# Kernel tuning notes

Hardware: AMD Instinct MI355X
Metric: run time of the kernel (lower is better)

The kernel has to match this reference:

```python
import jax, jax.numpy as jnp
import numpy as np

ALPHA = 0.5
EPS = 1e-12

def _l2norm(v):
    return v / (jnp.linalg.norm(v) + EPS)

def _spectral_norm_weight(W, u):
    # torch spectral_norm forward (training, n_power_iterations=1):
    # one power iteration with detached u, v; sigma = u' @ W @ v; W_sn = W / sigma
    v = jax.lax.stop_gradient(_l2norm(W.T @ u))          # [in]
    u2 = jax.lax.stop_gradient(_l2norm(W @ v))           # [out]
    sigma = u2 @ (W @ v)
    return W / sigma


def setup_inputs() -> dict:
    key = jax.random.key(0)
    ks = jax.random.split(key, 12)
    B, D_IN, D_H, D_OUT = 256, 1024, 2048, 1000

    def xavier(k, shape, gain):
        fan_out, fan_in = shape
        a = gain * np.sqrt(6.0 / (fan_in + fan_out))
        return jax.random.uniform(k, shape, jnp.float32, -a, a)

    x = jax.random.normal(ks[0], (B, D_IN), jnp.float32)
    # W_in: nn.Linear default init (kaiming-uniform-ish); plain uniform is fine for a reference
    lim_in = 1.0 / np.sqrt(D_IN)
    W_in_w = jax.random.uniform(ks[1], (D_H, D_IN), jnp.float32, -lim_in, lim_in)
    W_in_b = jax.random.uniform(ks[2], (D_H,), jnp.float32, -lim_in, lim_in)
    u = jax.random.normal(ks[3], (D_H,), jnp.float32)  # spectral-norm power-iteration vector

    W0 = xavier(ks[4], (D_H, D_H), 0.8)
    W1 = xavier(ks[5], (D_H, D_H), 0.8)
    W2 = xavier(ks[6], (D_H, D_H), 0.8)
    b0 = jnp.zeros((D_H,), jnp.float32)
    b1 = jnp.zeros((D_H,), jnp.float32)
    b2 = jnp.zeros((D_H,), jnp.float32)

    lim_h = 1.0 / np.sqrt(D_H)
    head_w = jax.random.uniform(ks[7], (D_OUT, D_H), jnp.float32, -lim_h, lim_h)
    head_b = jax.random.uniform(ks[8], (D_OUT,), jnp.float32, -lim_h, lim_h)

    return {"x": x, "W_in_w": W_in_w, "W_in_b": W_in_b, "u": u,
            "W0": W0, "b0": b0, "W1": W1, "b1": b1, "W2": W2, "b2": b2,
            "head_w": head_w, "head_b": head_b, "steps": 30}


def reference(x, W_in_w, W_in_b, u, W0, b0, W1, b1, W2, b2, head_w, head_b, steps):
    W_in_sn = _spectral_norm_weight(W_in_w, u)
    x_proj = x @ W_in_sn.T + W_in_b                      # [B, D_H], constant across steps
    layers = ((W0, b0), (W1, b1), (W2, b2))

    def step(h, _):
        for W, b in layers:
            h = (1.0 - ALPHA) * h + ALPHA * jnp.tanh(x_proj + h @ W.T + b)
        return h, None

    h0 = jnp.zeros((x.shape[0], W0.shape[0]), x.dtype)
    h, _ = jax.lax.scan(step, h0, None, length=steps)
    return h @ head_w.T + head_b
```

## Files before the change

### kernel.cpp

```cpp
#include <hip/hip_runtime.h>
#include <hip/hip_fp16.h>
#include <math.h>

typedef _Float16 h16;
typedef __attribute__((ext_vector_type(8))) _Float16 half8;
typedef __attribute__((ext_vector_type(4))) float f32x4;

#define GLOAD_LDS16(gp, lp) __builtin_amdgcn_global_load_lds( \
    (const __attribute__((address_space(1))) void*)(gp),      \
    (__attribute__((address_space(3))) void*)(lp), 16, 0, 0)

union SmemGemm3 {
  h16   buf[3][96 * 128];
  float red[4][2048];
};

__device__ __forceinline__ void stage3(SmemGemm3& sm, int bi,
                                       const h16* __restrict__ Ag,
                                       const h16* __restrict__ Bg,
                                       int kk, int kdim, int wave, int lane) {
  h16* As = sm.buf[bi];
  h16* Bs = As + 32 * 128;
  const int kb = kk * 128;
#pragma unroll
  for (int i = 0; i < 2; ++i) {
    const int id = wave * 2 + i;
    const int chunk = id * 64 + lane;
    const int r = chunk >> 4, cg = chunk & 15;
    GLOAD_LDS16(Ag + (long)r * kdim + kb + ((cg ^ (r & 7)) << 3),
                As + id * 512);
  }
#pragma unroll
  for (int i = 0; i < 4; ++i) {
    const int id = wave * 4 + i;
    const int chunk = id * 64 + lane;
    const int r = chunk >> 4, cg = chunk & 15;
    GLOAD_LDS16(Bg + (long)r * kdim + kb + ((cg ^ (r & 7)) << 3),
                Bs + id * 512);
  }
}

template <int KDIM>
__device__ __forceinline__ void gemm_core3(SmemGemm3& sm,
                                           const h16* __restrict__ Ag,
                                           const h16* __restrict__ Bg,
                                           int wave, int lane) {
  f32x4 acc[2][4];
#pragma unroll
  for (int a = 0; a < 2; ++a)
#pragma unroll
    for (int c = 0; c < 4; ++c) acc[a][c] = (f32x4){0.f, 0.f, 0.f, 0.f};

  const int mr = lane & 15, q = lane >> 4;
  const int kg = wave * 4 + q;
  const int ro = ((kg ^ (mr & 7)) << 3);
  constexpr int NIT = KDIM / 128;
  stage3(sm, 0, Ag, Bg, 0, KDIM, wave, lane);
  stage3(sm, 1, Ag, Bg, 1, KDIM, wave, lane);
#pragma unroll
  for (int kk = 0; kk < NIT; ++kk) {
    if (kk + 2 < NIT) {
      stage3(sm, (kk + 2) % 3, Ag, Bg, kk + 2, KDIM, wave, lane);
      asm volatile("s_waitcnt vmcnt(12)" ::: "memory");
    } else if (kk + 2 == NIT) {
      asm volatile("s_waitcnt vmcnt(6)" ::: "memory");
    } else {
      asm volatile("s_waitcnt vmcnt(0)" ::: "memory");
    }
    __builtin_amdgcn_s_barrier();
    const h16* As = sm.buf[kk % 3];
    const h16* Bs = As + 32 * 128;
    half8 a0 = *(const half8*)(As + mr * 128 + ro);
    half8 a1 = *(const half8*)(As + (mr + 16) * 128 + ro);
#pragma unroll
    for (int fc = 0; fc < 4; ++fc) {
      half8 bv = *(const half8*)(Bs + (fc * 16 + mr) * 128 + ro);
      acc[0][fc] = __builtin_amdgcn_mfma_f32_16x16x32_f16(a0, bv, acc[0][fc], 0, 0, 0);
      acc[1][fc] = __builtin_amdgcn_mfma_f32_16x16x32_f16(a1, bv, acc[1][fc], 0, 0, 0);
    }
    asm volatile("s_waitcnt lgkmcnt(0)" ::: "memory");
    __builtin_amdgcn_s_barrier();
  }
  __syncthreads();
#pragma unroll
  for (int fr = 0; fr < 2; ++fr)
#pragma unroll
    for (int fc = 0; fc < 4; ++fc)
#pragma unroll
      for (int r = 0; r < 4; ++r)
        sm.red[wave][(fr * 16 + q * 4 + r) * 64 + fc * 16 + mr] = acc[fr][fc][r];
  __syncthreads();
}

__device__ __forceinline__ float fast_tanh(float x) {
  float e = __expf(2.0f * fabsf(x));
  float t = 1.0f - 2.0f / (e + 1.0f);
  return copysignf(t, x);
}

__global__ void k_zero(float* tbuf, float* sbuf) {
  const int t = threadIdx.x;
  tbuf[t] = 0.f;
  if (t < 2) sbuf[t] = 0.f;
}

__global__ void __launch_bounds__(256)
k_prep1(const float* __restrict__ Win, const float* __restrict__ u,
        float* __restrict__ t) {
  const int kc = blockIdx.x & 3, jc = blockIdx.x >> 2;
  const int k = kc * 256 + threadIdx.x;
  const int j0 = jc * 64;
  float acc = 0.f;
#pragma unroll 4
  for (int j = 0; j < 64; ++j)
    acc = fmaf(Win[(long)(j0 + j) * 1024 + k], u[j0 + j], acc);
  atomicAdd(&t[k], acc);
}

__global__ void __launch_bounds__(256)
k_prep1b(const float* __restrict__ t, float* __restrict__ sbuf) {
  const int k = blockIdx.x * 256 + threadIdx.x;
  float v = t[k];
  float p = v * v;
#pragma unroll
  for (int off = 32; off > 0; off >>= 1) p += __shfl_down(p, off);
  if ((threadIdx.x & 63) == 0) atomicAdd(&sbuf[0], p);
}

__global__ void __launch_bounds__(256)
k_prep2(const float* __restrict__ Win, const float* __restrict__ t,
        float* __restrict__ sbuf) {
  const int row = blockIdx.x * 4 + (threadIdx.x >> 6);
  const int lane = threadIdx.x & 63;
  float acc = 0.f;
  for (int kk = lane; kk < 1024; kk += 64)
    acc = fmaf(Win[row * 1024 + kk], t[kk], acc);
#pragma unroll
  for (int off = 32; off > 0; off >>= 1) acc += __shfl_down(acc, off);
  if (lane == 0) atomicAdd(&sbuf[1], acc * acc);
}

__global__ void __launch_bounds__(256)
k_cvt(const float* __restrict__ W0, const float* __restrict__ W1,
      const float* __restrict__ W2, const float* __restrict__ Win,
      const float* __restrict__ Hw, const float* __restrict__ X,
      h16* __restrict__ w16, h16* __restrict__ wi16,
      h16* __restrict__ hw16, h16* __restrict__ x16) {
  const long e = (long)(blockIdx.x * 256 + threadIdx.x) * 8;
  const float* src; h16* dst;
  if (e < 4194304)       { src = W0 + e;              dst = w16 + e; }
  else if (e < 8388608)  { src = W1 + (e - 4194304);  dst = w16 + e; }
  else if (e < 12582912) { src = W2 + (e - 8388608);  dst = w16 + e; }
  else if (e < 14680064) { src = Win + (e - 12582912); dst = wi16 + (e - 12582912); }
  else if (e < 16728064) { src = Hw + (e - 14680064);  dst = hw16 + (e - 14680064); }
  else if (e < 16777216) {
    half8 z = (half8){};
    *(half8*)(hw16 + 2048000 + (e - 16728064)) = z;
    return;
  }
  else                   { src = X + (e - 16777216);   dst = x16 + (e - 16777216); }
  f32x4 f0 = *(const f32x4*)src, f1 = *(const f32x4*)(src + 4);
  half8 h;
#pragma unroll
  for (int i = 0; i < 4; ++i) { h[i] = (h16)f0[i]; h[i + 4] = (h16)f1[i]; }
  *(half8*)dst = h;
}

__global__ void __launch_bounds__(256)
k_xproj(const h16* __restrict__ x16, const h16* __restrict__ wi16,
        const float* __restrict__ Winb, const float* __restrict__ sbuf,
        float* __restrict__ xp, float* __restrict__ h32, h16* __restrict__ h16a) {
  __shared__ SmemGemm3 sm;
  const int rb = blockIdx.x >> 5, cb = blockIdx.x & 31;
  const int wave = threadIdx.x >> 6, lane = threadIdx.x & 63;
  gemm_core3<1024>(sm, x16 + rb * 32 * 1024, wi16 + (long)cb * 64 * 1024, wave, lane);
  const float inv_sigma = sqrtf(sbuf[0] / sbuf[1]);
  const int e = threadIdx.x * 8;
  const int gi = rb * 32 + (e >> 6), gj = cb * 64 + (e & 63);
  const long base = (long)gi * 2048 + gj;
  f32x4 s0 = *(const f32x4*)&sm.red[0][e], s1 = *(const f32x4*)&sm.red[0][e + 4];
#pragma unroll
  for (int w = 1; w < 4; ++w) {
    s0 += *(const f32x4*)&sm.red[w][e];
    s1 += *(const f32x4*)&sm.red[w][e + 4];
  }
  f32x4 b0v = *(const f32x4*)&Winb[gj], b1v = *(const f32x4*)&Winb[gj + 4];
  f32x4 v0 = s0 * inv_sigma + b0v, v1 = s1 * inv_sigma + b1v;
  *(f32x4*)&xp[base] = v0; *(f32x4*)&xp[base + 4] = v1;
  f32x4 zz = (f32x4){0.f, 0.f, 0.f, 0.f};
  *(f32x4*)&h32[base] = zz; *(f32x4*)&h32[base + 4] = zz;
  half8 hz = (half8){};
  *(half8*)&h16a[base] = hz;
}

__global__ void __launch_bounds__(256)
k_layer(const h16* __restrict__ hin, const h16* __restrict__ W,
        const float* __restrict__ bl, const float* __restrict__ xp,
        float* __restrict__ h32, h16* __restrict__ hout) {
  __shared__ SmemGemm3 sm;
  const int rb = blockIdx.x >> 5, cb = blockIdx.x & 31;
  const int wave = threadIdx.x >> 6, lane = threadIdx.x & 63;
  gemm_core3<2048>(sm, hin + rb * 32 * 2048, W + (long)cb * 64 * 2048, wave, lane);
  const int e = threadIdx.x * 8;
  const int gi = rb * 32 + (e >> 6), gj = cb * 64 + (e & 63);
  const long base = (long)gi * 2048 + gj;
  f32x4 s0 = *(const f32x4*)&sm.red[0][e], s1 = *(const f32x4*)&sm.red[0][e + 4];
#pragma unroll
  for (int w = 1; w < 4; ++w) {
    s0 += *(const f32x4*)&sm.red[w][e];
    s1 += *(const f32x4*)&sm.red[w][e + 4];
  }
  f32x4 xp0 = *(const f32x4*)&xp[base], xp1 = *(const f32x4*)&xp[base + 4];
  f32x4 b0v = *(const f32x4*)&bl[gj],   b1v = *(const f32x4*)&bl[gj + 4];
  f32x4 ho0 = *(const f32x4*)&h32[base], ho1 = *(const f32x4*)&h32[base + 4];
  f32x4 z0 = xp0 + s0 + b0v, z1 = xp1 + s1 + b1v;
  f32x4 hn0, hn1; half8 hh;
#pragma unroll
  for (int i = 0; i < 4; ++i) {
    hn0[i] = 0.5f * ho0[i] + 0.5f * fast_tanh(z0[i]);
    hn1[i] = 0.5f * ho1[i] + 0.5f * fast_tanh(z1[i]);
    hh[i] = (h16)hn0[i]; hh[i + 4] = (h16)hn1[i];
  }
  *(f32x4*)&h32[base] = hn0; *(f32x4*)&h32[base + 4] = hn1;
  *(half8*)&hout[base] = hh;
}

__global__ void __launch_bounds__(256)
k_head(const h16* __restrict__ hf, const h16* __restrict__ hw16,
       const float* __restrict__ hb, float* __restrict__ out) {
  __shared__ SmemGemm3 sm;
  const int rb = blockIdx.x >> 4, cb = blockIdx.x & 15;
  const int wave = threadIdx.x >> 6, lane = threadIdx.x & 63;
  gemm_core3<2048>(sm, hf + rb * 32 * 2048, hw16 + (long)cb * 64 * 2048, wave, lane);
  const int e = threadIdx.x * 8;
  const int gi = rb * 32 + (e >> 6), gj = cb * 64 + (e & 63);
  f32x4 s0 = *(const f32x4*)&sm.red[0][e], s1 = *(const f32x4*)&sm.red[0][e + 4];
#pragma unroll
  for (int w = 1; w < 4; ++w) {
    s0 += *(const f32x4*)&sm.red[w][e];
    s1 += *(const f32x4*)&sm.red[w][e + 4];
  }
#pragma unroll
  for (int i = 0; i < 4; ++i) {
    int j0 = gj + i;
    if (j0 < 1000) out[(long)gi * 1000 + j0] = s0[i] + hb[j0];
    int j1 = gj + 4 + i;
    if (j1 < 1000) out[(long)gi * 1000 + j1] = s1[i] + hb[j1];
  }
}

#define OFF_W16   0L
#define OFF_WI16  25165824L
#define OFF_X16   29360128L
#define OFF_HW16  29884416L
#define OFF_XP    34078720L
#define OFF_H32   36175872L
#define OFF_H16A  38273024L
#define OFF_H16B  39321600L
#define OFF_T     40370176L
#define OFF_S     40374272L

extern "C" void kernel_launch(void* const* d_in, const int* in_sizes, int n_in,
                              void* d_out, int out_size, void* d_ws, size_t ws_size,
                              hipStream_t stream) {
  const float* x     = (const float*)d_in[0];
  const float* Win_w = (const float*)d_in[1];
  const float* Win_b = (const float*)d_in[2];
  const float* u     = (const float*)d_in[3];
  const float* W0    = (const float*)d_in[4];
  const float* b0    = (const float*)d_in[5];
  const float* W1    = (const float*)d_in[6];
  const float* b1    = (const float*)d_in[7];
  const float* W2    = (const float*)d_in[8];
  const float* b2    = (const float*)d_in[9];
  const float* headw = (const float*)d_in[10];
  const float* headb = (const float*)d_in[11];

  char* ws = (char*)d_ws;
  h16*   w16  = (h16*)(ws + OFF_W16);
  h16*   wi16 = (h16*)(ws + OFF_WI16);
  h16*   x16  = (h16*)(ws + OFF_X16);
  h16*   hw16 = (h16*)(ws + OFF_HW16);
  float* xp   = (float*)(ws + OFF_XP);
  float* h32  = (float*)(ws + OFF_H32);
  h16*   h16a = (h16*)(ws + OFF_H16A);
  h16*   h16b = (h16*)(ws + OFF_H16B);
  float* tbuf = (float*)(ws + OFF_T);
  float* sbuf = (float*)(ws + OFF_S);

  k_zero<<<1, 1024, 0, stream>>>(tbuf, sbuf);
  k_prep1<<<128, 256, 0, stream>>>(Win_w, u, tbuf);
  k_prep1b<<<4, 256, 0, stream>>>(tbuf, sbuf);
  k_prep2<<<512, 256, 0, stream>>>(Win_w, tbuf, sbuf);
  k_cvt<<<8320, 256, 0, stream>>>(W0, W1, W2, Win_w, headw, x, w16, wi16, hw16, x16);
  k_xproj<<<256, 256, 0, stream>>>(x16, wi16, Win_b, sbuf, xp, h32, h16a);

  const h16*   wptr[3] = {w16, w16 + 4194304, w16 + 8388608};
  const float* bptr[3] = {b0, b1, b2};
  h16* hbuf[2] = {h16a, h16b};
  for (int s = 0; s < 30; ++s) {
    for (int l = 0; l < 3; ++l) {
      const int d = s * 3 + l;
      k_layer<<<256, 256, 0, stream>>>(hbuf[d & 1], wptr[l], bptr[l], xp, h32,
                                       hbuf[(d + 1) & 1]);
    }
  }
  k_head<<<128, 256, 0, stream>>>(hbuf[0], hw16, headb, (float*)d_out);
}
```

Measured before the change: 997.0 us.

## Fuse 90 layer launches into one persistent kernel with row-block barriers

Replaces 90 separate layer kernel launches with a single persistent kernel. Blocks sharing a 32-row batch slice synchronize through atomic counters in global memory, one counter per row block. The fp32 hidden state now stays in registers across steps instead of making a round trip through global memory, and the first layer skips its GEMM because h0 is zero. This removes launch overhead and the h32 traffic, but it relies on all 256 blocks being co-resident and adds spin-wait barrier costs.

```diff
diff --git a/kernel.cpp b/kernel.cpp
--- a/kernel.cpp
+++ b/kernel.cpp
@@ -98,10 +98,78 @@
   return copysignf(t, x);
 }
 
-__global__ void k_zero(float* tbuf, float* sbuf) {
+__global__ void __launch_bounds__(256)
+k_layers90(const h16* __restrict__ w16, const float* __restrict__ xp,
+           const float* __restrict__ b0v, const float* __restrict__ b1v,
+           const float* __restrict__ b2v, h16* __restrict__ ha,
+           h16* __restrict__ hb, unsigned* __restrict__ csync) {
+  __shared__ SmemGemm3 sm;
+  const int rb = blockIdx.x >> 5, cb = blockIdx.x & 31;
+  const int wave = threadIdx.x >> 6, lane = threadIdx.x & 63;
+  const int e = threadIdx.x * 8;
+  const int gi = rb * 32 + (e >> 6), gj = cb * 64 + (e & 63);
+  const long obase = (long)gi * 2048 + gj;
+  const f32x4 xpA = *(const f32x4*)&xp[obase];
+  const f32x4 xpB = *(const f32x4*)&xp[obase + 4];
+  f32x4 hA, hB;
+  half8 hh;
+
+  {
+    f32x4 z0 = xpA + *(const f32x4*)&b0v[gj];
+    f32x4 z1 = xpB + *(const f32x4*)&b0v[gj + 4];
+#pragma unroll
+    for (int i = 0; i < 4; ++i) {
+      hA[i] = 0.5f * fast_tanh(z0[i]);
+      hB[i] = 0.5f * fast_tanh(z1[i]);
+      hh[i] = (h16)hA[i]; hh[i + 4] = (h16)hB[i];
+    }
+    *(half8*)&hb[obase] = hh;
+  }
+
+#pragma unroll 1
+  for (int d = 1; d < 90; ++d) {
+    asm volatile("s_waitcnt vmcnt(0)" ::: "memory");
+    __syncthreads();
+    if (threadIdx.x == 0) {
+      __builtin_amdgcn_fence(__ATOMIC_RELEASE, "agent");
+      atomicAdd(&csync[rb], 1u);
+      while (__hip_atomic_load(&csync[rb], __ATOMIC_RELAXED,
+                               __HIP_MEMORY_SCOPE_AGENT) < (unsigned)(d * 32))
+        __builtin_amdgcn_s_sleep(2);
+      __builtin_amdgcn_fence(__ATOMIC_ACQUIRE, "agent");
+    }
+    __syncthreads();
+
+    const int L = d % 3;
+    const h16* W = w16 + (long)L * 4194304;
+    const float* bl = (L == 0) ? b0v : (L == 1) ? b1v : b2v;
+    const h16* hin = (d & 1) ? hb : ha;
+    h16* hout = (d & 1) ? ha : hb;
+    gemm_core3<2048>(sm, hin + rb * 32 * 2048, W + (long)cb * 64 * 2048,
+                     wave, lane);
+    f32x4 s0 = *(const f32x4*)&sm.red[0][e], s1 = *(const f32x4*)&sm.red[0][e + 4];
+#pragma unroll
+    for (int w = 1; w < 4; ++w) {
+      s0 += *(const f32x4*)&sm.red[w][e];
+      s1 += *(const f32x4*)&sm.red[w][e + 4];
+    }
+    f32x4 z0 = s0 + xpA + *(const f32x4*)&bl[gj];
+    f32x4 z1 = s1 + xpB + *(const f32x4*)&bl[gj + 4];
+#pragma unroll
+    for (int i = 0; i < 4; ++i) {
+      hA[i] = 0.5f * hA[i] + 0.5f * fast_tanh(z0[i]);
+      hB[i] = 0.5f * hB[i] + 0.5f * fast_tanh(z1[i]);
+      hh[i] = (h16)hA[i]; hh[i + 4] = (h16)hB[i];
+    }
+    *(half8*)&hout[obase] = hh;
+  }
+}
+
+__global__ void k_zero(float* tbuf, float* sbuf, unsigned* csync) {
   const int t = threadIdx.x;
   tbuf[t] = 0.f;
   if (t < 2) sbuf[t] = 0.f;
+  if (t < 8) csync[t] = 0u;
 }
 
 __global__ void __launch_bounds__(256)
@@ -169,7 +237,7 @@
 __global__ void __launch_bounds__(256)
 k_xproj(const h16* __restrict__ x16, const h16* __restrict__ wi16,
         const float* __restrict__ Winb, const float* __restrict__ sbuf,
-        float* __restrict__ xp, float* __restrict__ h32, h16* __restrict__ h16a) {
+        float* __restrict__ xp) {
   __shared__ SmemGemm3 sm;
   const int rb = blockIdx.x >> 5, cb = blockIdx.x & 31;
   const int wave = threadIdx.x >> 6, lane = threadIdx.x & 63;
@@ -187,42 +255,6 @@
   f32x4 b0v = *(const f32x4*)&Winb[gj], b1v = *(const f32x4*)&Winb[gj + 4];
   f32x4 v0 = s0 * inv_sigma + b0v, v1 = s1 * inv_sigma + b1v;
   *(f32x4*)&xp[base] = v0; *(f32x4*)&xp[base + 4] = v1;
-  f32x4 zz = (f32x4){0.f, 0.f, 0.f, 0.f};
-  *(f32x4*)&h32[base] = zz; *(f32x4*)&h32[base + 4] = zz;
-  half8 hz = (half8){};
-  *(half8*)&h16a[base] = hz;
-}
-
-__global__ void __launch_bounds__(256)
-k_layer(const h16* __restrict__ hin, const h16* __restrict__ W,
-        const float* __restrict__ bl, const float* __restrict__ xp,
-        float* __restrict__ h32, h16* __restrict__ hout) {
-  __shared__ SmemGemm3 sm;
-  const int rb = blockIdx.x >> 5, cb = blockIdx.x & 31;
-  const int wave = threadIdx.x >> 6, lane = threadIdx.x & 63;
-  gemm_core3<2048>(sm, hin + rb * 32 * 2048, W + (long)cb * 64 * 2048, wave, lane);
-  const int e = threadIdx.x * 8;
-  const int gi = rb * 32 + (e >> 6), gj = cb * 64 + (e & 63);
-  const long base = (long)gi * 2048 + gj;
-  f32x4 s0 = *(const f32x4*)&sm.red[0][e], s1 = *(const f32x4*)&sm.red[0][e + 4];
-#pragma unroll
-  for (int w = 1; w < 4; ++w) {
-    s0 += *(const f32x4*)&sm.red[w][e];
-    s1 += *(const f32x4*)&sm.red[w][e + 4];
-  }
-  f32x4 xp0 = *(const f32x4*)&xp[base], xp1 = *(const f32x4*)&xp[base + 4];
-  f32x4 b0v = *(const f32x4*)&bl[gj],   b1v = *(const f32x4*)&bl[gj + 4];
-  f32x4 ho0 = *(const f32x4*)&h32[base], ho1 = *(const f32x4*)&h32[base + 4];
-  f32x4 z0 = xp0 + s0 + b0v, z1 = xp1 + s1 + b1v;
-  f32x4 hn0, hn1; half8 hh;
-#pragma unroll
-  for (int i = 0; i < 4; ++i) {
-    hn0[i] = 0.5f * ho0[i] + 0.5f * fast_tanh(z0[i]);
-    hn1[i] = 0.5f * ho1[i] + 0.5f * fast_tanh(z1[i]);
-    hh[i] = (h16)hn0[i]; hh[i + 4] = (h16)hn1[i];
-  }
-  *(f32x4*)&h32[base] = hn0; *(f32x4*)&h32[base + 4] = hn1;
-  *(half8*)&hout[base] = hh;
 }
 
 __global__ void __launch_bounds__(256)
@@ -254,11 +286,11 @@
 #define OFF_X16   29360128L
 #define OFF_HW16  29884416L
 #define OFF_XP    34078720L
-#define OFF_H32   36175872L
-#define OFF_H16A  38273024L
-#define OFF_H16B  39321600L
-#define OFF_T     40370176L
-#define OFF_S     40374272L
+#define OFF_H16A  36175872L
+#define OFF_H16B  37224448L
+#define OFF_T     38273024L
+#define OFF_S     38277120L
+#define OFF_SYNC  38277136L
 
 extern "C" void kernel_launch(void* const* d_in, const int* in_sizes, int n_in,
                               void* d_out, int out_size, void* d_ws, size_t ws_size,
@@ -277,33 +309,23 @@
   const float* headb = (const float*)d_in[11];
 
   char* ws = (char*)d_ws;
-  h16*   w16  = (h16*)(ws + OFF_W16);
-  h16*   wi16 = (h16*)(ws + OFF_WI16);
-  h16*   x16  = (h16*)(ws + OFF_X16);
-  h16*   hw16 = (h16*)(ws + OFF_HW16);
-  float* xp   = (float*)(ws + OFF_XP);
-  float* h32  = (float*)(ws + OFF_H32);
-  h16*   h16a = (h16*)(ws + OFF_H16A);
-  h16*   h16b = (h16*)(ws + OFF_H16B);
-  float* tbuf = (float*)(ws + OFF_T);
-  float* sbuf = (float*)(ws + OFF_S);
-
-  k_zero<<<1, 1024, 0, stream>>>(tbuf, sbuf);
+  h16*      w16   = (h16*)(ws + OFF_W16);
+  h16*      wi16  = (h16*)(ws + OFF_WI16);
+  h16*      x16   = (h16*)(ws + OFF_X16);
+  h16*      hw16  = (h16*)(ws + OFF_HW16);
+  float*    xp    = (float*)(ws + OFF_XP);
+  h16*      h16a  = (h16*)(ws + OFF_H16A);
+  h16*      h16b  = (h16*)(ws + OFF_H16B);
+  float*    tbuf  = (float*)(ws + OFF_T);
+  float*    sbuf  = (float*)(ws + OFF_S);
+  unsigned* csync = (unsigned*)(ws + OFF_SYNC);
+
+  k_zero<<<1, 1024, 0, stream>>>(tbuf, sbuf, csync);
   k_prep1<<<128, 256, 0, stream>>>(Win_w, u, tbuf);
   k_prep1b<<<4, 256, 0, stream>>>(tbuf, sbuf);
   k_prep2<<<512, 256, 0, stream>>>(Win_w, tbuf, sbuf);
   k_cvt<<<8320, 256, 0, stream>>>(W0, W1, W2, Win_w, headw, x, w16, wi16, hw16, x16);
-  k_xproj<<<256, 256, 0, stream>>>(x16, wi16, Win_b, sbuf, xp, h32, h16a);
-
-  const h16*   wptr[3] = {w16, w16 + 4194304, w16 + 8388608};
-  const float* bptr[3] = {b0, b1, b2};
-  h16* hbuf[2] = {h16a, h16b};
-  for (int s = 0; s < 30; ++s) {
-    for (int l = 0; l < 3; ++l) {
-      const int d = s * 3 + l;
-      k_layer<<<256, 256, 0, stream>>>(hbuf[d & 1], wptr[l], bptr[l], xp, h32,
-                                       hbuf[(d + 1) & 1]);
-    }
-  }
-  k_head<<<128, 256, 0, stream>>>(hbuf[0], hw16, headb, (float*)d_out);
-}
+  k_xproj<<<256, 256, 0, stream>>>(x16, wi16, Win_b, sbuf, xp);
+  k_layers90<<<256, 256, 0, stream>>>(w16, xp, b0, b1, b2, h16a, h16b, csync);
+  k_head<<<128, 256, 0, stream>>>(h16a, hw16, headb, (float*)d_out);
+}
```

After: 2.408 ms. +141.6%, slower.
